# Kernel tuning notes

Measured on AMD Instinct MI355X. Metric: run time of the kernel, lower is better.

The kernel has to match this reference:

```python
import jax, jax.numpy as jnp
import numpy as np

EPS = 1e-5

def _layernorm(x, g, b):
    mu = jnp.mean(x, axis=-1, keepdims=True)
    var = jnp.mean(jnp.square(x - mu), axis=-1, keepdims=True)
    return (x - mu) * jax.lax.rsqrt(var + EPS) * g + b

def _mlp(x, w1, b1, w2, b2):
    h = jax.nn.gelu(jnp.einsum('bnd,dh->bnh', x, w1) + b1, approximate=False)
    return jnp.einsum('bnh,hd->bnd', h, w2) + b2

def setup_inputs() -> dict:
    key = jax.random.key(0)
    B, N, D, H = 2, 8192, 1024, 4096
    ks = jax.random.split(key, 12)
    s1 = 1.0 / np.sqrt(D)
    s2 = 1.0 / np.sqrt(H)
    return {
        'x': jax.random.normal(ks[0], (B, N, D), dtype=jnp.float32),
        'mask': jax.random.randint(ks[1], (B, N), 0, 2) > 0,
        'g_rgb': jnp.ones((D,), jnp.float32),
        'b_rgb': jnp.zeros((D,), jnp.float32),
        'w1_rgb': jax.random.normal(ks[2], (D, H), dtype=jnp.float32) * s1,
        'b1_rgb': jnp.zeros((H,), jnp.float32),
        'w2_rgb': jax.random.normal(ks[3], (H, D), dtype=jnp.float32) * s2,
        'b2_rgb': jnp.zeros((D,), jnp.float32),
        'g_expr': jnp.ones((D,), jnp.float32),
        'b_expr': jnp.zeros((D,), jnp.float32),
        'w1_expr': jax.random.normal(ks[4], (D, H), dtype=jnp.float32) * s1,
        'b1_expr': jnp.zeros((H,), jnp.float32),
        'w2_expr': jax.random.normal(ks[5], (H, D), dtype=jnp.float32) * s2,
        'b2_expr': jnp.zeros((D,), jnp.float32),
    }

def reference(x, mask, g_rgb, b_rgb, w1_rgb, b1_rgb, w2_rgb, b2_rgb,
              g_expr, b_expr, w1_expr, b1_expr, w2_expr, b2_expr):
    # Per-token routing: rgb expert where mask, expr expert where ~mask.
    # LayerNorm+MLP are pointwise per token, so dense compute + select is
    # mathematically identical to the torch gather->compute->scatter.
    z_rgb = _mlp(_layernorm(x, g_rgb, b_rgb), w1_rgb, b1_rgb, w2_rgb, b2_rgb)
    z_expr = _mlp(_layernorm(x, g_expr, b_expr), w1_expr, b1_expr, w2_expr, b2_expr)
    z = jnp.where(mask[..., None], z_rgb, z_expr)
    return z.astype(jnp.float16)  # torch scatters into a float16 buffer
```

## Files before the change

kernel.cpp:

```cpp
#include <hip/hip_runtime.h>
#include <hip/hip_bf16.h>
#include <hip/hip_fp16.h>

#define D_ 1024
#define H_ 4096
#define NTOK 16384
#define MPAD 16512

typedef __attribute__((ext_vector_type(8))) short bf16x8;
typedef __attribute__((ext_vector_type(4))) float f32x4;

static __device__ __forceinline__ unsigned short f2bf(float f) {
  union { float f; unsigned u; } x; x.f = f;
  unsigned u = x.u + 0x7fffu + ((x.u >> 16) & 1u);
  return (unsigned short)(u >> 16);
}

static __device__ __forceinline__ void gld16(const void* g, void* l) {
  __builtin_amdgcn_global_load_lds(
      (const __attribute__((address_space(1))) unsigned int*)g,
      (__attribute__((address_space(3))) unsigned int*)l, 16, 0, 0);
}

__global__ __launch_bounds__(256) void transpose_bf16_kernel(
    const float* __restrict__ src, unsigned short* __restrict__ dst, int R, int C) {
  __shared__ float tile[32][33];
  const int c0 = blockIdx.x * 32, r0 = blockIdx.y * 32;
  const int tx = threadIdx.x & 31, ty = threadIdx.x >> 5;
#pragma unroll
  for (int i = 0; i < 32; i += 8)
    tile[ty + i][tx] = src[(size_t)(r0 + ty + i) * C + c0 + tx];
  __syncthreads();
#pragma unroll
  for (int i = 0; i < 32; i += 8)
    dst[(size_t)(c0 + ty + i) * R + r0 + tx] = f2bf(tile[tx][ty + i]);
}

__global__ __launch_bounds__(256) void compact_kernel(
    const int* __restrict__ mask, int* __restrict__ perm, int* __restrict__ counts) {
  const int NT = 256, CH = NTOK / NT;
  __shared__ int sm[NTOK];
  __shared__ int wsum[4];
  const int t = threadIdx.x;
  const int ln = t & 63, wv = t >> 6;
  for (int i = t; i < NTOK; i += NT) sm[i] = mask[i];
  for (int i = t; i < MPAD; i += NT) perm[i] = -1;
  __syncthreads();
  const int base = t * CH;
  int cnt = 0;
  for (int i = 0; i < CH; ++i) cnt += (sm[base + i] != 0);
  int sc = cnt;
#pragma unroll
  for (int o = 1; o < 64; o <<= 1) {
    int u = __shfl_up(sc, o, 64);
    if (ln >= o) sc += u;
  }
  if (ln == 63) wsum[wv] = sc;
  __syncthreads();
  int woff = 0;
#pragma unroll
  for (int j = 0; j < 4; ++j) woff += (j < wv) ? wsum[j] : 0;
  const int total1 = wsum[0] + wsum[1] + wsum[2] + wsum[3];
  if (t == 0) { counts[0] = total1; counts[1] = NTOK - total1; }
  const int excl = woff + sc - cnt;
  const int expr_base = ((total1 + 127) >> 7) << 7;
  int p1 = excl;
  int p0 = expr_base + (base - excl);
  for (int i = 0; i < CH; ++i) {
    const int idx = base + i;
    if (sm[idx] != 0) perm[p1++] = idx; else perm[p0++] = idx;
  }
}

__global__ __launch_bounds__(256) void ln_kernel(
    const float* __restrict__ x, const int* __restrict__ mask,
    const int* __restrict__ perm,
    const float* __restrict__ g_rgb, const float* __restrict__ b_rgb,
    const float* __restrict__ g_expr, const float* __restrict__ b_expr,
    unsigned short* __restrict__ xln) {
  const int i = blockIdx.x;
  const int t = perm[i];
  if (t < 0) return;
  const int tid = threadIdx.x;
  const float4 v = ((const float4*)(x + (size_t)t * D_))[tid];
  float s = v.x + v.y + v.z + v.w;
  float ss = v.x * v.x + v.y * v.y + v.z * v.z + v.w * v.w;
#pragma unroll
  for (int o = 32; o > 0; o >>= 1) {
    s += __shfl_xor(s, o, 64);
    ss += __shfl_xor(ss, o, 64);
  }
  __shared__ float red[8];
  const int wv = tid >> 6, ln = tid & 63;
  if (ln == 0) { red[wv] = s; red[4 + wv] = ss; }
  __syncthreads();
  s = red[0] + red[1] + red[2] + red[3];
  ss = red[4] + red[5] + red[6] + red[7];
  const float mu = s * (1.0f / D_);
  const float var = ss * (1.0f / D_) - mu * mu;
  const float rs = rsqrtf(var + 1e-5f);
  const bool rgb = mask[t] != 0;
  const float4 gv = ((const float4*)(rgb ? g_rgb : g_expr))[tid];
  const float4 bv = ((const float4*)(rgb ? b_rgb : b_expr))[tid];
  const unsigned short o0 = f2bf((v.x - mu) * rs * gv.x + bv.x);
  const unsigned short o1 = f2bf((v.y - mu) * rs * gv.y + bv.y);
  const unsigned short o2 = f2bf((v.z - mu) * rs * gv.z + bv.z);
  const unsigned short o3 = f2bf((v.w - mu) * rs * gv.w + bv.w);
  uint2 pk;
  pk.x = (unsigned)o0 | ((unsigned)o1 << 16);
  pk.y = (unsigned)o2 | ((unsigned)o3 << 16);
  *((uint2*)(xln + (size_t)i * D_ + tid * 4)) = pk;
}

template <int EP, int K, int N>
__global__ __launch_bounds__(256) void gemm_kernel(
    const unsigned short* __restrict__ A,
    const unsigned short* __restrict__ Wt_rgb,
    const unsigned short* __restrict__ Wt_expr,
    const float* __restrict__ bias_rgb,
    const float* __restrict__ bias_expr,
    const int* __restrict__ counts,
    const int* __restrict__ perm,
    void* __restrict__ OutP) {
  constexpr int BM = 128, BN = 128, BK = 64;
  constexpr int MT = MPAD / BM;
  constexpr int NT = N / BN;
  const int tid = threadIdx.x;
  const int id = blockIdx.x;
  const int xcd = id & 7;
  const int slot = id >> 3;
  const int p = xcd * ((MT * NT) / 8) + slot;
  const int m0 = (p / NT) * BM;
  const int n0 = (p % NT) * BN;
  const int cnt_rgb = counts[0];
  const unsigned short* Wt = (m0 < cnt_rgb) ? Wt_rgb : Wt_expr;
  const float* bias = (m0 < cnt_rgb) ? bias_rgb : bias_expr;

  __shared__ unsigned short As[BM * BK];
  __shared__ unsigned short Bs[BN * BK];

  f32x4 acc[4][4] = {};

  const unsigned short* Abase = A + (size_t)m0 * K;
  const unsigned short* Bbase = Wt + (size_t)n0 * K;
  const int lane = tid & 63, wave = tid >> 6;
  const int wm = (wave & 1) * 64, wn = (wave >> 1) * 64;
  const int quad = lane >> 4, l16 = lane & 15;

  for (int k0 = 0; k0 < K; k0 += BK) {
#pragma unroll
    for (int it = 0; it < 4; ++it) {
      const int s = it * 256 + tid;
      const int row = s >> 3;
      const int ks = ((s ^ row) & 7) * 8;
      gld16(Abase + (size_t)row * K + k0 + ks, (char*)As + s * 16);
      gld16(Bbase + (size_t)row * K + k0 + ks, (char*)Bs + s * 16);
    }
    __syncthreads();
#pragma unroll
    for (int kk = 0; kk < BK; kk += 32) {
      const int cbase = (kk >> 3) + quad;
      bf16x8 a[4], b[4];
#pragma unroll
      for (int mi = 0; mi < 4; ++mi) {
        const int row = wm + mi * 16 + l16;
        a[mi] = *(const bf16x8*)(As + row * BK + (((cbase ^ row) & 7) << 3));
      }
#pragma unroll
      for (int ni = 0; ni < 4; ++ni) {
        const int row = wn + ni * 16 + l16;
        b[ni] = *(const bf16x8*)(Bs + row * BK + (((cbase ^ row) & 7) << 3));
      }
#pragma unroll
      for (int mi = 0; mi < 4; ++mi)
#pragma unroll
        for (int ni = 0; ni < 4; ++ni)
          acc[mi][ni] = __builtin_amdgcn_mfma_f32_16x16x32_bf16(a[mi], b[ni], acc[mi][ni], 0, 0, 0);
    }
    __syncthreads();
  }

  float bv[4];
#pragma unroll
  for (int ni = 0; ni < 4; ++ni) bv[ni] = bias[n0 + wn + ni * 16 + l16];

#pragma unroll
  for (int mi = 0; mi < 4; ++mi) {
#pragma unroll
    for (int r = 0; r < 4; ++r) {
      const int row = m0 + wm + mi * 16 + quad * 4 + r;
      if (EP == 0) {
        unsigned short* orow = (unsigned short*)OutP + (size_t)row * N + n0 + wn + l16;
#pragma unroll
        for (int ni = 0; ni < 4; ++ni) {
          float v = acc[mi][ni][r] + bv[ni];
          v = 0.5f * v * (1.0f + erff(v * 0.70710678118654752f));
          orow[ni * 16] = f2bf(v);
        }
      } else {
        const int p2 = perm[row];
        if (p2 < 0) continue;
        float* orow = (float*)OutP + (size_t)p2 * N + n0 + wn + l16;
#pragma unroll
        for (int ni = 0; ni < 4; ++ni) {
          float v = acc[mi][ni][r] + bv[ni];
          orow[ni * 16] = __half2float(__float2half_rn(v));
        }
      }
    }
  }
}

extern "C" void kernel_launch(void* const* d_in, const int* in_sizes, int n_in,
                              void* d_out, int out_size, void* d_ws, size_t ws_size,
                              hipStream_t stream) {
  const float* x       = (const float*)d_in[0];
  const int*   mask    = (const int*)d_in[1];
  const float* g_rgb   = (const float*)d_in[2];
  const float* b_rgb   = (const float*)d_in[3];
  const float* w1_rgb  = (const float*)d_in[4];
  const float* b1_rgb  = (const float*)d_in[5];
  const float* w2_rgb  = (const float*)d_in[6];
  const float* b2_rgb  = (const float*)d_in[7];
  const float* g_expr  = (const float*)d_in[8];
  const float* b_expr  = (const float*)d_in[9];
  const float* w1_expr = (const float*)d_in[10];
  const float* b1_expr = (const float*)d_in[11];
  const float* w2_expr = (const float*)d_in[12];
  const float* b2_expr = (const float*)d_in[13];

  char* w = (char*)d_ws;
  int* counts               = (int*)(w + 0);
  int* perm                 = (int*)(w + 256);
  unsigned short* w1t_rgb   = (unsigned short*)(w + 66560);
  unsigned short* w1t_expr  = (unsigned short*)(w + 8455168);
  unsigned short* w2t_rgb   = (unsigned short*)(w + 16843776);
  unsigned short* w2t_expr  = (unsigned short*)(w + 25232384);
  unsigned short* xln       = (unsigned short*)(w + 33620992);
  unsigned short* h         = (unsigned short*)(w + 67437568);

  transpose_bf16_kernel<<<dim3(H_ / 32, D_ / 32), 256, 0, stream>>>(w1_rgb, w1t_rgb, D_, H_);
  transpose_bf16_kernel<<<dim3(H_ / 32, D_ / 32), 256, 0, stream>>>(w1_expr, w1t_expr, D_, H_);
  transpose_bf16_kernel<<<dim3(D_ / 32, H_ / 32), 256, 0, stream>>>(w2_rgb, w2t_rgb, H_, D_);
  transpose_bf16_kernel<<<dim3(D_ / 32, H_ / 32), 256, 0, stream>>>(w2_expr, w2t_expr, H_, D_);

  compact_kernel<<<1, 256, 0, stream>>>(mask, perm, counts);

  ln_kernel<<<MPAD, 256, 0, stream>>>(x, mask, perm, g_rgb, b_rgb, g_expr, b_expr, xln);

  gemm_kernel<0, D_, H_><<<dim3((H_ / 128) * (MPAD / 128)), 256, 0, stream>>>(
      xln, w1t_rgb, w1t_expr, b1_rgb, b1_expr, counts, perm, h);

  gemm_kernel<1, H_, D_><<<dim3((D_ / 128) * (MPAD / 128)), 256, 0, stream>>>(
      h, w2t_rgb, w2t_expr, b2_rgb, b2_expr, counts, perm, d_out);
}
```

Before: 700.3 us.

## Merge weight transposes, precompute GEMM addresses, use tanh-form sigmoid GELU

Folds the four weight-transpose launches into one kernel that picks its source by block index. In the GEMM it precomputes the global and LDS pointers once and advances them by BK each iteration, instead of recomputing swizzled offsets inside the loop. It also swaps the exact erf GELU for a tanh-style approximation built from exp and a reciprocal, which lowers epilogue cost at some accuracy risk.

```diff
diff --git a/kernel.cpp b/kernel.cpp
--- a/kernel.cpp
+++ b/kernel.cpp
@@ -22,10 +22,25 @@
       (__attribute__((address_space(3))) unsigned int*)l, 16, 0, 0);
 }
 
-__global__ __launch_bounds__(256) void transpose_bf16_kernel(
-    const float* __restrict__ src, unsigned short* __restrict__ dst, int R, int C) {
+static __device__ __forceinline__ float gelu_fast(float x) {
+  const float z = x * (1.5957691216f + 0.0713548163f * x * x);
+  return x * __builtin_amdgcn_rcpf(1.0f + __expf(-z));
+}
+
+__global__ __launch_bounds__(256) void transpose4_kernel(
+    const float* __restrict__ w1r, const float* __restrict__ w1e,
+    const float* __restrict__ w2r, const float* __restrict__ w2e,
+    unsigned short* __restrict__ o1r, unsigned short* __restrict__ o1e,
+    unsigned short* __restrict__ o2r, unsigned short* __restrict__ o2e) {
   __shared__ float tile[32][33];
-  const int c0 = blockIdx.x * 32, r0 = blockIdx.y * 32;
+  const int t = blockIdx.x;
+  const float* src; unsigned short* dst; int R, C, tl;
+  if (t < 4096)       { src = w1r; dst = o1r; R = D_; C = H_; tl = t; }
+  else if (t < 8192)  { src = w1e; dst = o1e; R = D_; C = H_; tl = t - 4096; }
+  else if (t < 12288) { src = w2r; dst = o2r; R = H_; C = D_; tl = t - 8192; }
+  else                { src = w2e; dst = o2e; R = H_; C = D_; tl = t - 12288; }
+  const int tc = C >> 5;
+  const int r0 = (tl / tc) * 32, c0 = (tl % tc) * 32;
   const int tx = threadIdx.x & 31, ty = threadIdx.x >> 5;
 #pragma unroll
   for (int i = 0; i < 32; i += 8)
@@ -141,36 +156,57 @@
 
   f32x4 acc[4][4] = {};
 
-  const unsigned short* Abase = A + (size_t)m0 * K;
-  const unsigned short* Bbase = Wt + (size_t)n0 * K;
   const int lane = tid & 63, wave = tid >> 6;
   const int wm = (wave & 1) * 64, wn = (wave >> 1) * 64;
   const int quad = lane >> 4, l16 = lane & 15;
 
+  const unsigned short* ag[4];
+  const unsigned short* bg[4];
+  char* al[4];
+  char* bl[4];
+#pragma unroll
+  for (int it = 0; it < 4; ++it) {
+    const int s = it * 256 + tid;
+    const int row = s >> 3;
+    const int ks = ((s ^ row) & 7) * 8;
+    ag[it] = A + (size_t)(m0 + row) * K + ks;
+    bg[it] = Wt + (size_t)(n0 + row) * K + ks;
+    al[it] = (char*)As + s * 16;
+    bl[it] = (char*)Bs + s * 16;
+  }
+  const unsigned short* ap[2][4];
+  const unsigned short* bp[2][4];
+#pragma unroll
+  for (int hh = 0; hh < 2; ++hh) {
+    const int cb = hh * 4 + quad;
+#pragma unroll
+    for (int mi = 0; mi < 4; ++mi) {
+      const int row = wm + mi * 16 + l16;
+      ap[hh][mi] = As + row * BK + (((cb ^ row) & 7) << 3);
+    }
+#pragma unroll
+    for (int ni = 0; ni < 4; ++ni) {
+      const int row = wn + ni * 16 + l16;
+      bp[hh][ni] = Bs + row * BK + (((cb ^ row) & 7) << 3);
+    }
+  }
+
   for (int k0 = 0; k0 < K; k0 += BK) {
 #pragma unroll
     for (int it = 0; it < 4; ++it) {
-      const int s = it * 256 + tid;
-      const int row = s >> 3;
-      const int ks = ((s ^ row) & 7) * 8;
-      gld16(Abase + (size_t)row * K + k0 + ks, (char*)As + s * 16);
-      gld16(Bbase + (size_t)row * K + k0 + ks, (char*)Bs + s * 16);
+      gld16(ag[it], al[it]);
+      gld16(bg[it], bl[it]);
+      ag[it] += BK;
+      bg[it] += BK;
     }
     __syncthreads();
 #pragma unroll
-    for (int kk = 0; kk < BK; kk += 32) {
-      const int cbase = (kk >> 3) + quad;
+    for (int hh = 0; hh < 2; ++hh) {
       bf16x8 a[4], b[4];
 #pragma unroll
-      for (int mi = 0; mi < 4; ++mi) {
-        const int row = wm + mi * 16 + l16;
-        a[mi] = *(const bf16x8*)(As + row * BK + (((cbase ^ row) & 7) << 3));
-      }
-#pragma unroll
-      for (int ni = 0; ni < 4; ++ni) {
-        const int row = wn + ni * 16 + l16;
-        b[ni] = *(const bf16x8*)(Bs + row * BK + (((cbase ^ row) & 7) << 3));
-      }
+      for (int mi = 0; mi < 4; ++mi) a[mi] = *(const bf16x8*)ap[hh][mi];
+#pragma unroll
+      for (int ni = 0; ni < 4; ++ni) b[ni] = *(const bf16x8*)bp[hh][ni];
 #pragma unroll
       for (int mi = 0; mi < 4; ++mi)
 #pragma unroll
@@ -193,9 +229,7 @@
         unsigned short* orow = (unsigned short*)OutP + (size_t)row * N + n0 + wn + l16;
 #pragma unroll
         for (int ni = 0; ni < 4; ++ni) {
-          float v = acc[mi][ni][r] + bv[ni];
-          v = 0.5f * v * (1.0f + erff(v * 0.70710678118654752f));
-          orow[ni * 16] = f2bf(v);
+          orow[ni * 16] = f2bf(gelu_fast(acc[mi][ni][r] + bv[ni]));
         }
       } else {
         const int p2 = perm[row];
@@ -239,12 +273,10 @@
   unsigned short* xln       = (unsigned short*)(w + 33620992);
   unsigned short* h         = (unsigned short*)(w + 67437568);
 
-  transpose_bf16_kernel<<<dim3(H_ / 32, D_ / 32), 256, 0, stream>>>(w1_rgb, w1t_rgb, D_, H_);
-  transpose_bf16_kernel<<<dim3(H_ / 32, D_ / 32), 256, 0, stream>>>(w1_expr, w1t_expr, D_, H_);
-  transpose_bf16_kernel<<<dim3(D_ / 32, H_ / 32), 256, 0, stream>>>(w2_rgb, w2t_rgb, H_, D_);
-  transpose_bf16_kernel<<<dim3(D_ / 32, H_ / 32), 256, 0, stream>>>(w2_expr, w2t_expr, H_, D_);
-
   compact_kernel<<<1, 256, 0, stream>>>(mask, perm, counts);
+
+  transpose4_kernel<<<16384, 256, 0, stream>>>(
+      w1_rgb, w1_expr, w2_rgb, w2_expr, w1t_rgb, w1t_expr, w2t_rgb, w2t_expr);
 
   ln_kernel<<<MPAD, 256, 0, stream>>>(x, mask, perm, g_rgb, b_rgb, g_expr, b_expr, xln);
 
```

New measurement: 600.2 us. -14.3%, faster.
